# Kernel tuning notes

Measured on AMD Instinct MI355X. Metric: run time of the kernel, lower is better.

Reference implementation:

```python
import jax, jax.numpy as jnp
import numpy as np

ALPHA = 0.2  # LeakyReLU negative slope
NEG_INF = -1e9


def setup_inputs() -> dict:
    key = jax.random.key(0)
    k1, k2, k3, k4 = jax.random.split(key, 4)
    B, N, IN, OUT = 8, 2048, 512, 32
    graph_input = jax.random.normal(k1, (B, N, IN), dtype=jnp.float32)
    adj = jax.random.randint(k2, (B, N, N), 0, 2, dtype=jnp.int32)
    W_fc = jax.random.normal(k3, (OUT, IN), dtype=jnp.float32) * (1.0 / np.sqrt(IN))
    W_attn = jax.random.normal(k4, (1, 2 * OUT), dtype=jnp.float32) * (1.0 / np.sqrt(2 * OUT))
    return {"graph_input": graph_input, "adj": adj, "W_fc": W_fc, "W_attn": W_attn}


def reference(graph_input, adj, W_fc, W_attn):
    # h: [B, N, 32]
    h = jnp.einsum('bni,oi->bno', graph_input, W_fc)
    out_dim = W_fc.shape[0]
    # attn_fc(cat(h_i, h_j)) is separable: a1.h_i + a2.h_j
    a1 = W_attn[0, :out_dim]   # [32]
    a2 = W_attn[0, out_dim:]   # [32]
    f1 = jnp.einsum('bno,o->bn', h, a1)  # [B, N]
    f2 = jnp.einsum('bno,o->bn', h, a2)  # [B, N]
    scores = jax.nn.leaky_relu(f1[:, :, None] + f2[:, None, :], negative_slope=ALPHA)  # [B,N,N]
    scores = jnp.where(adj == 0, NEG_INF, scores)
    attn = jax.nn.softmax(scores, axis=2)
    # NOTE: original multiplies attention with graph_input (not h)
    h_prime = jnp.einsum('bnm,bmi->bni', attn, graph_input)  # [B, N, IN]
    return jax.nn.elu(h_prime)  # concat=True path
```

## Files before the change

### kernel.cpp

```cpp
#include <hip/hip_runtime.h>
#include <hip/hip_bf16.h>

#define BATCH 8
#define NN    2048
#define FIN   512
#define FOUT  32
#define GALPHA 0.2f
#define NROW  64
#define NIT   32

typedef float  f32x4  __attribute__((ext_vector_type(4)));
typedef __bf16 bf16x8 __attribute__((ext_vector_type(8)));
typedef unsigned short u16;
typedef u16 u16x8 __attribute__((ext_vector_type(8)));

static __device__ __forceinline__ u16 f2bf(float f) {
    __hip_bfloat16 h = __float2bfloat16(f);
    union { __hip_bfloat16 h; u16 u; } c; c.h = h; return c.u;
}
static __device__ __forceinline__ float bf2f(u16 u) {
    union { u16 u; __hip_bfloat16 h; } c; c.u = u; return __bfloat162float(c.h);
}

__global__ __launch_bounds__(256) void k_prep(
    const float* __restrict__ x, const int* __restrict__ adj,
    const float* __restrict__ Wfc, const float* __restrict__ Wat,
    __hip_bfloat16* __restrict__ xt,
    float* __restrict__ f1, float* __restrict__ f2,
    unsigned int* __restrict__ bits)
{
    const int bx = blockIdx.x;
    const int it = bx & 7, mt = (bx >> 3) & 31, b = bx >> 8;
    const int m0 = mt * 64, i0 = it * 64;
    const int tt = threadIdx.x;

    __shared__ __align__(16) char smem[16384];
    u16 (*tile)[72]   = (u16(*)[72])smem;
    float* w1s        = (float*)(smem + 9216);
    float* w2s        = (float*)(smem + 9216 + 256);
    unsigned int* pls = (unsigned int*)smem;

    if (tt < 64) {
        const int i = i0 + tt;
        float s1 = 0.f, s2 = 0.f;
        #pragma unroll
        for (int o = 0; o < FOUT; o++) {
            float wv = Wfc[o * FIN + i];
            s1 += wv * Wat[o];
            s2 += wv * Wat[FOUT + o];
        }
        w1s[tt] = s1; w2s[tt] = s2;
    }
    __syncthreads();

    const int mm  = tt >> 3;
    const int icl = (tt & 7) * 8;
    const float* xb = x + ((size_t)b * NN + m0) * FIN + i0;
    f32x4 wA = *(const f32x4*)&w1s[icl];
    f32x4 wB = *(const f32x4*)&w1s[icl + 4];
    f32x4 wC = *(const f32x4*)&w2s[icl];
    f32x4 wD = *(const f32x4*)&w2s[icl + 4];
    float p1[2], p2[2];
    #pragma unroll
    for (int h = 0; h < 2; h++) {
        int m = mm + h * 32;
        const f32x4* src = (const f32x4*)(xb + (size_t)m * FIN + icl);
        f32x4 v0 = src[0], v1 = src[1];
        u16x8 pk;
        float s1 = 0.f, s2 = 0.f;
        #pragma unroll
        for (int j = 0; j < 4; j++) {
            pk[j] = f2bf(v0[j]); pk[4 + j] = f2bf(v1[j]);
            s1 += v0[j] * wA[j] + v1[j] * wB[j];
            s2 += v0[j] * wC[j] + v1[j] * wD[j];
        }
        p1[h] = s1; p2[h] = s2;
        *(u16x8*)&tile[m][icl] = pk;
    }
    #pragma unroll
    for (int off = 1; off < 8; off <<= 1) {
        p1[0] += __shfl_xor(p1[0], off); p1[1] += __shfl_xor(p1[1], off);
        p2[0] += __shfl_xor(p2[0], off); p2[1] += __shfl_xor(p2[1], off);
    }
    if ((tt & 7) == 0) {
        size_t r0 = (size_t)b * NN + m0 + mm;
        atomicAdd(&f1[r0], p1[0]);      atomicAdd(&f1[r0 + 32], p1[1]);
        atomicAdd(&f2[r0], p2[0]);      atomicAdd(&f2[r0 + 32], p2[1]);
    }
    __syncthreads();
    __hip_bfloat16* xtb = xt + ((size_t)b * FIN + i0) * NN + m0;
    const int mc = (tt & 7) * 8;
    #pragma unroll
    for (int h = 0; h < 2; h++) {
        int ii = (tt >> 3) + h * 32;
        u16x8 v;
        #pragma unroll
        for (int j = 0; j < 8; j++) v[j] = tile[mc + j][ii];
        *(u16x8*)(xtb + (size_t)ii * NN + mc) = v;
    }

    __syncthreads();
    {
        const int* ab = adj + (size_t)(b * NN + m0 + it * 8) * NN;
        #pragma unroll
        for (int s = 0; s < 16; s++) {
            int4 v = *(const int4*)(ab + (size_t)(s * 256 + tt) * 4);
            unsigned int pb = (v.x != 0 ? 0x00000001u : 0u)
                            | (v.y != 0 ? 0x00000100u : 0u)
                            | (v.z != 0 ? 0x00010000u : 0u)
                            | (v.w != 0 ? 0x01000000u : 0u);
            pls[s * 256 + tt] = pb;
        }
        __syncthreads();
        const int r = tt >> 5, c0 = tt & 31;
        #pragma unroll
        for (int half = 0; half < 2; half++) {
            const int c = c0 + half * 32;
            const unsigned int* q = pls + r * 512 + c * 8;
            unsigned int bv = 0;
            #pragma unroll
            for (int j = 0; j < 8; j++) {
                unsigned int pb = q[j];
                bv |= (pb         & 1u) << (j * 4 + 0);
                bv |= ((pb >> 8)  & 1u) << (j * 4 + 1);
                bv |= ((pb >> 16) & 1u) << (j * 4 + 2);
                bv |= ((pb >> 24) & 1u) << (j * 4 + 3);
            }
            bits[(size_t)(b * NN + m0 + it * 8 + r) * 64 + c] = bv;
        }
    }
}

__global__ __launch_bounds__(512, 4) void k_main(
    const unsigned int* __restrict__ bits, const __hip_bfloat16* __restrict__ xt,
    const float* __restrict__ f1, const float* __restrict__ f2,
    float* __restrict__ out)
{
    const int bx = blockIdx.x;
    const int b = bx & 7, rt = (bx >> 3) & 31, it = bx >> 8;
    const int n0 = rt * NROW;
    const int i0 = it * 256;
    const int tid = threadIdx.x;
    const int lane = tid & 63, wv = tid >> 6;
    const int quad = lane >> 4, l15 = lane & 15;

    __shared__ u16 At[2][NROW * 64];
    __shared__ float rs[NROW];

    const int grow = tid >> 3;
    const int q8   = tid & 7;
    const unsigned char* bp = (const unsigned char*)bits
                              + ((size_t)(b * NN) + n0 + grow) * 256 + q8;
    const float* f2p = f2 + b * NN + q8 * 8;
    const float  f1v = f1[b * NN + n0 + grow];
    const int swz = grow & 7;
    u16* wp0 = &At[0][grow * 64 + ((q8 ^ swz) * 8)];
    float rpart = 0.f;

    const __hip_bfloat16* xtp = xt + ((size_t)(b * FIN) + i0 + wv * 32 + l15) * NN + quad * 8;

    f32x4 acc[4][2];
    #pragma unroll
    for (int s = 0; s < 4; s++) { acc[s][0] = (f32x4){0,0,0,0}; acc[s][1] = (f32x4){0,0,0,0}; }

    auto gen = [&](int buf, unsigned int bv, const f32x4* fr) {
        u16x8 pk0;
        #pragma unroll
        for (int e = 0; e < 8; e++) {
            float s  = f1v + fr[e >> 2][e & 3];
            float ls = fmaxf(s, GALPHA * s);
            float ev = ((bv >> e) & 1u) ? __expf(ls) : 0.f;
            u16 hb = f2bf(ev);
            rpart += bf2f(hb);
            pk0[e] = hb;
        }
        *(u16x8*)(wp0 + buf * (NROW * 64)) = pk0;
    };

    {
        unsigned int b0 = bp[0];
        f32x4 g0[2];
        #pragma unroll
        for (int j = 0; j < 2; j++) g0[j] = *(const f32x4*)(f2p + j * 4);
        gen(0, b0, g0);
    }
    unsigned int brng[2];
    f32x4 frng[2][2];
    brng[1] = bp[8];
    #pragma unroll
    for (int j = 0; j < 2; j++) frng[1][j] = *(const f32x4*)(f2p + 64 + j * 4);
    brng[0] = bp[16];
    #pragma unroll
    for (int j = 0; j < 2; j++) frng[0][j] = *(const f32x4*)(f2p + 128 + j * 4);

    bf16x8 Bc[2][2], Bn[2][2];
    #pragma unroll
    for (int ks = 0; ks < 2; ks++)
        #pragma unroll
        for (int c = 0; c < 2; c++)
            Bc[ks][c] = *(const bf16x8*)(xtp + ks * 32 + (size_t)(c * 16) * NN);
    __syncthreads();

    #pragma unroll 2
    for (int t = 0; t < NIT; t++) {
        const int cur = t & 1;
        if (t < NIT - 1) {
            const __hip_bfloat16* xk = xtp + (t + 1) * 64;
            #pragma unroll
            for (int ks = 0; ks < 2; ks++)
                #pragma unroll
                for (int c = 0; c < 2; c++)
                    Bn[ks][c] = *(const bf16x8*)(xk + ks * 32 + (size_t)(c * 16) * NN);
        }
        #pragma unroll
        for (int ks = 0; ks < 2; ks++) {
            #pragma unroll
            for (int s = 0; s < 4; s++) {
                const int row = s * 16 + l15;
                bf16x8 Af = *(const bf16x8*)&At[cur][row * 64 + (((ks * 4 + quad) ^ (row & 7)) * 8)];
                acc[s][0] = __builtin_amdgcn_mfma_f32_16x16x32_bf16(Af, Bc[ks][0], acc[s][0], 0, 0, 0);
                acc[s][1] = __builtin_amdgcn_mfma_f32_16x16x32_bf16(Af, Bc[ks][1], acc[s][1], 0, 0, 0);
            }
        }
        if (t < NIT - 1) {
            gen(1 - cur, brng[(t + 1) & 1], frng[(t + 1) & 1]);
            if (t < NIT - 2) {
                brng[t & 1] = bp[(t + 2) * 8];
                #pragma unroll
                for (int j = 0; j < 2; j++)
                    frng[t & 1][j] = *(const f32x4*)(f2p + (t + 2) * 64 + j * 4);
            }
        }
        asm volatile("s_waitcnt lgkmcnt(0)\ns_barrier" ::: "memory");
        #pragma unroll
        for (int ks = 0; ks < 2; ks++) {
            Bc[ks][0] = Bn[ks][0]; Bc[ks][1] = Bn[ks][1];
        }
    }

    rpart += __shfl_xor(rpart, 1);
    rpart += __shfl_xor(rpart, 2);
    rpart += __shfl_xor(rpart, 4);
    if (q8 == 0) rs[grow] = 1.0f / rpart;
    __syncthreads();

    #pragma unroll
    for (int s = 0; s < 4; s++) {
        #pragma unroll
        for (int r = 0; r < 4; r++) {
            const int row = s * 16 + quad * 4 + r;
            const float inv = rs[row];
            float* op = out + ((size_t)b * NN + (n0 + row)) * FIN + i0 + wv * 32 + l15;
            #pragma unroll
            for (int c = 0; c < 2; c++) {
                float v = acc[s][c][r] * inv;
                v = v > 0.f ? v : (__expf(v) - 1.f);
                op[c * 16] = v;
            }
        }
    }
}

extern "C" void kernel_launch(void* const* d_in, const int* in_sizes, int n_in,
                              void* d_out, int out_size, void* d_ws, size_t ws_size,
                              hipStream_t stream) {
    const float* x   = (const float*)d_in[0];
    const int*   adj = (const int*)d_in[1];
    const float* Wfc = (const float*)d_in[2];
    const float* Wat = (const float*)d_in[3];
    float* out = (float*)d_out;

    float* f1 = (float*)d_ws;
    float* f2 = f1 + BATCH * NN;
    unsigned int* bits = (unsigned int*)(f2 + BATCH * NN);
    __hip_bfloat16* xt = (__hip_bfloat16*)(bits + (size_t)BATCH * NN * 64);

    hipMemsetAsync(f1, 0, (size_t)2 * BATCH * NN * sizeof(float), stream);
    hipLaunchKernelGGL(k_prep, dim3(2048), dim3(256), 0, stream,
                       x, adj, Wfc, Wat, xt, f1, f2, bits);
    hipLaunchKernelGGL(k_main, dim3(512),  dim3(512), 0, stream,
                       bits, xt, f1, f2, out);
}
```

Before: 299.6 us.

## Generate attention A-fragments in registers per wave, dropping LDS staging and barriers

Each wave now computes its own 16-row attention-weight fragment directly in registers and feeds it to MFMA. This removes the shared-memory double buffer, the per-iteration barrier, and the LDS reads. Blocks are retiled to 128 rows by 128 output features, and each wave loads 8 B fragments straight from global memory. The cost is that B tiles are reloaded by every wave without overlap or prefetching, the exp work is recomputed across 4 feature tiles instead of 2, and occupancy is lowered to 3 blocks per SIMD.

Measured after the change: 485.6 us. 1.62x slower.

```diff
diff --git a/kernel.cpp b/kernel.cpp
--- a/kernel.cpp
+++ b/kernel.cpp
@@ -6,7 +6,6 @@
 #define FIN   512
 #define FOUT  32
 #define GALPHA 0.2f
-#define NROW  64
 #define NIT   32
 
 typedef float  f32x4  __attribute__((ext_vector_type(4)));
@@ -131,132 +130,89 @@
     }
 }
 
-__global__ __launch_bounds__(512, 4) void k_main(
+__global__ __launch_bounds__(512, 3) void k_main(
     const unsigned int* __restrict__ bits, const __hip_bfloat16* __restrict__ xt,
     const float* __restrict__ f1, const float* __restrict__ f2,
     float* __restrict__ out)
 {
     const int bx = blockIdx.x;
-    const int b = bx & 7, rt = (bx >> 3) & 31, it = bx >> 8;
-    const int n0 = rt * NROW;
-    const int i0 = it * 256;
+    const int b = bx & 7, rt = (bx >> 3) & 15, it = bx >> 7;
+    const int n0 = rt * 128;
+    const int i0 = it * 128;
     const int tid = threadIdx.x;
     const int lane = tid & 63, wv = tid >> 6;
     const int quad = lane >> 4, l15 = lane & 15;
 
-    __shared__ u16 At[2][NROW * 64];
-    __shared__ float rs[NROW];
-
-    const int grow = tid >> 3;
-    const int q8   = tid & 7;
-    const unsigned char* bp = (const unsigned char*)bits
-                              + ((size_t)(b * NN) + n0 + grow) * 256 + q8;
-    const float* f2p = f2 + b * NN + q8 * 8;
-    const float  f1v = f1[b * NN + n0 + grow];
-    const int swz = grow & 7;
-    u16* wp0 = &At[0][grow * 64 + ((q8 ^ swz) * 8)];
+    const int row = n0 + wv * 16 + l15;
+    const float f1v = f1[b * NN + row];
+    const uint2* bpr = (const uint2*)((const unsigned char*)bits
+                                      + ((size_t)(b * NN) + row) * 256);
+    const float* f2b = f2 + b * NN + quad * 8;
+    const __hip_bfloat16* xtp = xt + ((size_t)(b * FIN) + i0 + l15) * NN + quad * 8;
+
+    f32x4 acc[8];
+    #pragma unroll
+    for (int c = 0; c < 8; c++) acc[c] = (f32x4){0, 0, 0, 0};
+
     float rpart = 0.f;
 
-    const __hip_bfloat16* xtp = xt + ((size_t)(b * FIN) + i0 + wv * 32 + l15) * NN + quad * 8;
-
-    f32x4 acc[4][2];
-    #pragma unroll
-    for (int s = 0; s < 4; s++) { acc[s][0] = (f32x4){0,0,0,0}; acc[s][1] = (f32x4){0,0,0,0}; }
-
-    auto gen = [&](int buf, unsigned int bv, const f32x4* fr) {
-        u16x8 pk0;
-        #pragma unroll
-        for (int e = 0; e < 8; e++) {
-            float s  = f1v + fr[e >> 2][e & 3];
-            float ls = fmaxf(s, GALPHA * s);
-            float ev = ((bv >> e) & 1u) ? __expf(ls) : 0.f;
-            u16 hb = f2bf(ev);
-            rpart += bf2f(hb);
-            pk0[e] = hb;
-        }
-        *(u16x8*)(wp0 + buf * (NROW * 64)) = pk0;
-    };
-
-    {
-        unsigned int b0 = bp[0];
-        f32x4 g0[2];
-        #pragma unroll
-        for (int j = 0; j < 2; j++) g0[j] = *(const f32x4*)(f2p + j * 4);
-        gen(0, b0, g0);
-    }
-    unsigned int brng[2];
-    f32x4 frng[2][2];
-    brng[1] = bp[8];
-    #pragma unroll
-    for (int j = 0; j < 2; j++) frng[1][j] = *(const f32x4*)(f2p + 64 + j * 4);
-    brng[0] = bp[16];
-    #pragma unroll
-    for (int j = 0; j < 2; j++) frng[0][j] = *(const f32x4*)(f2p + 128 + j * 4);
-
-    bf16x8 Bc[2][2], Bn[2][2];
-    #pragma unroll
-    for (int ks = 0; ks < 2; ks++)
-        #pragma unroll
-        for (int c = 0; c < 2; c++)
-            Bc[ks][c] = *(const bf16x8*)(xtp + ks * 32 + (size_t)(c * 16) * NN);
-    __syncthreads();
+    uint2 bv_n = bpr[0];
+    f32x4 f2n0 = *(const f32x4*)(f2b);
+    f32x4 f2n1 = *(const f32x4*)(f2b + 4);
+    f32x4 f2n2 = *(const f32x4*)(f2b + 32);
+    f32x4 f2n3 = *(const f32x4*)(f2b + 36);
 
     #pragma unroll 2
     for (int t = 0; t < NIT; t++) {
-        const int cur = t & 1;
+        const uint2 bw = bv_n;
+        const f32x4 fA = f2n0, fB = f2n1, fC = f2n2, fD = f2n3;
         if (t < NIT - 1) {
-            const __hip_bfloat16* xk = xtp + (t + 1) * 64;
-            #pragma unroll
-            for (int ks = 0; ks < 2; ks++)
-                #pragma unroll
-                for (int c = 0; c < 2; c++)
-                    Bn[ks][c] = *(const bf16x8*)(xk + ks * 32 + (size_t)(c * 16) * NN);
+            bv_n = bpr[t + 1];
+            const float* fp = f2b + (t + 1) * 64;
+            f2n0 = *(const f32x4*)(fp);
+            f2n1 = *(const f32x4*)(fp + 4);
+            f2n2 = *(const f32x4*)(fp + 32);
+            f2n3 = *(const f32x4*)(fp + 36);
         }
         #pragma unroll
         for (int ks = 0; ks < 2; ks++) {
-            #pragma unroll
-            for (int s = 0; s < 4; s++) {
-                const int row = s * 16 + l15;
-                bf16x8 Af = *(const bf16x8*)&At[cur][row * 64 + (((ks * 4 + quad) ^ (row & 7)) * 8)];
-                acc[s][0] = __builtin_amdgcn_mfma_f32_16x16x32_bf16(Af, Bc[ks][0], acc[s][0], 0, 0, 0);
-                acc[s][1] = __builtin_amdgcn_mfma_f32_16x16x32_bf16(Af, Bc[ks][1], acc[s][1], 0, 0, 0);
+            const __hip_bfloat16* xk = xtp + t * 64 + ks * 32;
+            bf16x8 Bf[8];
+            #pragma unroll
+            for (int c = 0; c < 8; c++)
+                Bf[c] = *(const bf16x8*)(xk + (size_t)(c * 16) * NN);
+            const unsigned int byte = ((ks ? bw.y : bw.x) >> (quad * 8)) & 0xffu;
+            const f32x4 f0 = ks ? fC : fA;
+            const f32x4 f1r = ks ? fD : fB;
+            union { u16x8 u; bf16x8 h; } a;
+            #pragma unroll
+            for (int e = 0; e < 8; e++) {
+                float s  = f1v + (e < 4 ? f0[e & 3] : f1r[e & 3]);
+                float ls = fmaxf(s, GALPHA * s);
+                float ev = ((byte >> e) & 1u) ? __expf(ls) : 0.f;
+                u16 hb = f2bf(ev);
+                rpart += bf2f(hb);
+                a.u[e] = hb;
             }
-        }
-        if (t < NIT - 1) {
-            gen(1 - cur, brng[(t + 1) & 1], frng[(t + 1) & 1]);
-            if (t < NIT - 2) {
-                brng[t & 1] = bp[(t + 2) * 8];
-                #pragma unroll
-                for (int j = 0; j < 2; j++)
-                    frng[t & 1][j] = *(const f32x4*)(f2p + (t + 2) * 64 + j * 4);
-            }
-        }
-        asm volatile("s_waitcnt lgkmcnt(0)\ns_barrier" ::: "memory");
-        #pragma unroll
-        for (int ks = 0; ks < 2; ks++) {
-            Bc[ks][0] = Bn[ks][0]; Bc[ks][1] = Bn[ks][1];
-        }
-    }
-
-    rpart += __shfl_xor(rpart, 1);
-    rpart += __shfl_xor(rpart, 2);
-    rpart += __shfl_xor(rpart, 4);
-    if (q8 == 0) rs[grow] = 1.0f / rpart;
-    __syncthreads();
-
-    #pragma unroll
-    for (int s = 0; s < 4; s++) {
-        #pragma unroll
-        for (int r = 0; r < 4; r++) {
-            const int row = s * 16 + quad * 4 + r;
-            const float inv = rs[row];
-            float* op = out + ((size_t)b * NN + (n0 + row)) * FIN + i0 + wv * 32 + l15;
-            #pragma unroll
-            for (int c = 0; c < 2; c++) {
-                float v = acc[s][c][r] * inv;
-                v = v > 0.f ? v : (__expf(v) - 1.f);
-                op[c * 16] = v;
-            }
+            #pragma unroll
+            for (int c = 0; c < 8; c++)
+                acc[c] = __builtin_amdgcn_mfma_f32_16x16x32_bf16(a.h, Bf[c], acc[c], 0, 0, 0);
+        }
+    }
+
+    rpart += __shfl_xor(rpart, 16);
+    rpart += __shfl_xor(rpart, 32);
+    const float inv = 1.0f / rpart;
+
+    #pragma unroll
+    for (int r = 0; r < 4; r++) {
+        const float invr = __shfl(inv, quad * 4 + r);
+        float* op = out + ((size_t)b * NN + n0 + wv * 16 + quad * 4 + r) * FIN + i0 + l15;
+        #pragma unroll
+        for (int c = 0; c < 8; c++) {
+            float v = acc[c][r] * invr;
+            v = v > 0.f ? v : (__expf(v) - 1.f);
+            op[c * 16] = v;
         }
     }
 }
```
